# Optimization experiments

Hardware: AMD Instinct MI355X
Metric: run time of the kernel (lower is better)

Reference implementation:

```python
import jax, jax.numpy as jnp
import numpy as np

B, S, H, I = 2, 2048, 4096, 16384
EPS = 1e-12


def setup_inputs() -> dict:
    key = jax.random.key(0)
    ks = jax.random.split(key, 8)
    w_scale = 0.02
    return {
        "input": jax.random.normal(ks[0], (B, S, H), jnp.float32),
        "residual": jax.random.normal(ks[1], (B, S, H), jnp.float32),
        "bias": jax.random.normal(ks[2], (H,), jnp.float32) * w_scale,
        "attn_nw": jnp.ones((H,), jnp.float32),
        "attn_nb": jnp.zeros((H,), jnp.float32),
        "inter_w": jax.random.normal(ks[3], (I, H), jnp.float32) * w_scale,
        "inter_b": jax.random.normal(ks[4], (I,), jnp.float32) * w_scale,
        "output_w": jax.random.normal(ks[5], (H, I), jnp.float32) * w_scale,
        "output_b": jax.random.normal(ks[6], (H,), jnp.float32) * w_scale,
    }


def reference(input, residual, bias, attn_nw, attn_nb, inter_w, inter_b, output_w, output_b):
    # Fused mlp_gemm: residual_add = input + residual + attn-output bias
    residual_add = input + residual + bias  # [B,S,H]
    # LayerNorm over hidden dim with attn_nw/attn_nb
    mean = jnp.mean(residual_add, axis=-1, keepdims=True)
    var = jnp.var(residual_add, axis=-1, keepdims=True)
    ln = (residual_add - mean) * jax.lax.rsqrt(var + EPS) * attn_nw + attn_nb
    # Intermediate GEMM + bias + GELU (DeepSpeed uses tanh-approx gelu)
    inter = jax.nn.gelu(jnp.einsum("bsh,ih->bsi", ln, inter_w) + inter_b, approximate=True)
    # Output projection (vector_matmul)
    out = jnp.einsum("bsi,hi->bsh", inter, output_w)
    # bias_residual: add residual_add and output bias
    return out + residual_add + output_b
```

## Files before the change

### kernel.cpp

```cpp
#include <hip/hip_runtime.h>
#include <hip/hip_bf16.h>
#include <cstdint>
#include <math.h>

typedef __attribute__((ext_vector_type(4))) float f32x4;
typedef __attribute__((ext_vector_type(8))) __bf16 bf16x8;

__device__ __forceinline__ unsigned short f2bf(float f) {
    union { float f; unsigned u; } v; v.f = f;
    unsigned u = v.u + 0x7fffu + ((v.u >> 16) & 1u);
    return (unsigned short)(u >> 16);
}

__device__ __forceinline__ float gelu_tanh(float x) {
    float x3 = x * x * x;
    float t = tanhf(0.7978845608028654f * (x + 0.044715f * x3));
    return 0.5f * x * (1.0f + t);
}

__device__ __forceinline__ void gload_lds16(const void* g, void* l) {
    __builtin_amdgcn_global_load_lds(
        (__attribute__((address_space(1))) void*)(uintptr_t)g,
        (__attribute__((address_space(3))) void*)(unsigned)(uintptr_t)l,
        16, 0, 0);
}

__global__ __launch_bounds__(256)
void fused_add_ln(const float* __restrict__ in, const float* __restrict__ res,
                  const float* __restrict__ bias, const float* __restrict__ nw,
                  const float* __restrict__ nb, float* __restrict__ resadd,
                  unsigned short* __restrict__ lnout, int H) {
    const int row = blockIdx.x;
    const int tid = threadIdx.x;
    const size_t base = (size_t)row * H;
    float v[16];
    float s = 0.f, ss = 0.f;
#pragma unroll
    for (int i = 0; i < 4; ++i) {
        int idx = (i * 256 + tid) * 4;
        float4 a = *(const float4*)(in + base + idx);
        float4 b = *(const float4*)(res + base + idx);
        float4 c = *(const float4*)(bias + idx);
        float x0 = a.x + b.x + c.x, x1 = a.y + b.y + c.y;
        float x2 = a.z + b.z + c.z, x3 = a.w + b.w + c.w;
        v[i * 4 + 0] = x0; v[i * 4 + 1] = x1; v[i * 4 + 2] = x2; v[i * 4 + 3] = x3;
        s += x0 + x1 + x2 + x3;
        ss += x0 * x0 + x1 * x1 + x2 * x2 + x3 * x3;
    }
#pragma unroll
    for (int off = 32; off > 0; off >>= 1) {
        s += __shfl_down(s, off);
        ss += __shfl_down(ss, off);
    }
    __shared__ float red[8];
    const int w = tid >> 6;
    if ((tid & 63) == 0) { red[w] = s; red[4 + w] = ss; }
    __syncthreads();
    s = red[0] + red[1] + red[2] + red[3];
    ss = red[4] + red[5] + red[6] + red[7];
    const float mean = s / H;
    const float var = ss / H - mean * mean;
    const float rstd = rsqrtf(var + 1e-12f);
#pragma unroll
    for (int i = 0; i < 4; ++i) {
        int idx = (i * 256 + tid) * 4;
        float4 wv = *(const float4*)(nw + idx);
        float4 bv = *(const float4*)(nb + idx);
        float4 r;
        r.x = v[i * 4 + 0]; r.y = v[i * 4 + 1]; r.z = v[i * 4 + 2]; r.w = v[i * 4 + 3];
        *(float4*)(resadd + base + idx) = r;
        ushort4 o;
        o.x = f2bf((r.x - mean) * rstd * wv.x + bv.x);
        o.y = f2bf((r.y - mean) * rstd * wv.y + bv.y);
        o.z = f2bf((r.z - mean) * rstd * wv.z + bv.z);
        o.w = f2bf((r.w - mean) * rstd * wv.w + bv.w);
        *(ushort4*)(lnout + base + idx) = o;
    }
}

__global__ __launch_bounds__(256)
void cast_w(const float* __restrict__ w, unsigned short* __restrict__ o, long long n4) {
    long long i = (long long)blockIdx.x * 256 + threadIdx.x;
    if (i >= n4) return;
    float4 f = *(const float4*)(w + i * 4);
    ushort4 u;
    u.x = f2bf(f.x); u.y = f2bf(f.y); u.z = f2bf(f.z); u.w = f2bf(f.w);
    *(ushort4*)(o + i * 4) = u;
}

#define GBM 256
#define GBN 256
#define GBK 64

template <int EPI>
__global__ __launch_bounds__(512, 2)
void gemm256(const unsigned short* __restrict__ A,
             const unsigned short* __restrict__ B,
             const float* __restrict__ bias_n,
             const float* __restrict__ resadd,
             void* __restrict__ Cout,
             int M, int N, int K) {
    __shared__ unsigned short lds[2][2][GBM * GBK];
    const int tid = threadIdx.x;
    const int lane = tid & 63;
    const int w = tid >> 6;
    const int wr = w >> 2;
    const int wc = w & 3;

    const int nwg = gridDim.x;
    const int lg = (blockIdx.x & 7) * (nwg >> 3) + (blockIdx.x >> 3);
    const int nbx = N / GBN;
    const int brow = lg / nbx;
    const int bcol = lg % nbx;

    const int srow = tid >> 3;
    const int scol = ((((tid & 7) << 4) ^ ((srow & 7) << 4)) >> 1);
    const unsigned short* srcA = A + (size_t)(brow * GBM + srow) * K + scol;
    const unsigned short* srcB = B + (size_t)(bcol * GBN + srow) * K + scol;
    char* ldsBase = (char*)&lds[0][0][0];
    const int dOff = tid * 16;

    f32x4 acc[8][4] = {};

    const int NT = K / GBK;

#pragma unroll
    for (int c = 0; c < 4; ++c) {
        gload_lds16(srcA + (size_t)(c * 64) * K, ldsBase + c * 8192 + dOff);
        gload_lds16(srcB + (size_t)(c * 64) * K, ldsBase + 32768 + c * 8192 + dOff);
    }

    const int lrow = lane & 15;
    const int lswz = (lane & 7) << 4;
    const int lkx = (lane >> 4) << 4;

    for (int t = 0; t < NT; ++t) {
        const int cur = t & 1;
        if (t + 1 < NT) {
            const int kt = (t + 1) * GBK;
            char* dst = ldsBase + (cur ^ 1) * 65536;
#pragma unroll
            for (int c = 0; c < 4; ++c) {
                gload_lds16(srcA + (size_t)(c * 64) * K + kt, dst + c * 8192 + dOff);
                gload_lds16(srcB + (size_t)(c * 64) * K + kt, dst + 32768 + c * 8192 + dOff);
            }
            asm volatile("s_waitcnt vmcnt(8)" ::: "memory");
        } else {
            asm volatile("s_waitcnt vmcnt(0)" ::: "memory");
        }
        asm volatile("s_barrier" ::: "memory");

        const char* sA = (const char*)ldsBase + cur * 65536;
        const char* sB = sA + 32768;

        bf16x8 bq[4][2];
#pragma unroll
        for (int ni = 0; ni < 4; ++ni)
#pragma unroll
            for (int kk = 0; kk < 2; ++kk)
                bq[ni][kk] = *(const bf16x8*)(sB
                    + ((wc * 64 + ni * 16 + lrow) << 7)
                    + (((kk << 6) | lkx) ^ lswz));

#pragma unroll
        for (int q = 0; q < 4; ++q) {
            bf16x8 aq[2][2];
#pragma unroll
            for (int m2 = 0; m2 < 2; ++m2)
#pragma unroll
                for (int kk = 0; kk < 2; ++kk)
                    aq[m2][kk] = *(const bf16x8*)(sA
                        + ((wr * 128 + (q * 2 + m2) * 16 + lrow) << 7)
                        + (((kk << 6) | lkx) ^ lswz));
            asm volatile("s_waitcnt lgkmcnt(0)" ::: "memory");
            __builtin_amdgcn_sched_barrier(0);
            __builtin_amdgcn_s_setprio(1);
#pragma unroll
            for (int m2 = 0; m2 < 2; ++m2)
#pragma unroll
                for (int ni = 0; ni < 4; ++ni)
#pragma unroll
                    for (int kk = 0; kk < 2; ++kk)
                        acc[q * 2 + m2][ni] = __builtin_amdgcn_mfma_f32_16x16x32_bf16(
                            aq[m2][kk], bq[ni][kk], acc[q * 2 + m2][ni], 0, 0, 0);
            __builtin_amdgcn_s_setprio(0);
            asm volatile("s_barrier" ::: "memory");
        }
    }

    const int c0 = bcol * GBN + wc * 64 + lrow;
    const int r0 = brow * GBM + wr * 128 + (lane >> 4) * 4;
#pragma unroll
    for (int mi = 0; mi < 8; ++mi) {
#pragma unroll
        for (int j = 0; j < 4; ++j) {
            const int row = r0 + mi * 16 + j;
#pragma unroll
            for (int ni = 0; ni < 4; ++ni) {
                const int col = c0 + ni * 16;
                float x = acc[mi][ni][j] + bias_n[col];
                if (EPI == 0) {
                    ((unsigned short*)Cout)[(size_t)row * N + col] = f2bf(gelu_tanh(x));
                } else {
                    const size_t off = (size_t)row * N + col;
                    ((float*)Cout)[off] = x + resadd[off];
                }
            }
        }
    }
}

extern "C" void kernel_launch(void* const* d_in, const int* in_sizes, int n_in,
                              void* d_out, int out_size, void* d_ws, size_t ws_size,
                              hipStream_t stream) {
    const float* input    = (const float*)d_in[0];
    const float* residual = (const float*)d_in[1];
    const float* bias     = (const float*)d_in[2];
    const float* attn_nw  = (const float*)d_in[3];
    const float* attn_nb  = (const float*)d_in[4];
    const float* inter_w  = (const float*)d_in[5];
    const float* inter_b  = (const float*)d_in[6];
    const float* output_w = (const float*)d_in[7];
    const float* output_b = (const float*)d_in[8];

    const int H = in_sizes[3];
    const int I = in_sizes[6];
    const int T = in_sizes[0] / H;

    char* ws = (char*)d_ws;
    float* resadd      = (float*)ws;
    unsigned short* ln = (unsigned short*)(ws + (size_t)T * H * 4);
    unsigned short* w1 = (unsigned short*)((char*)ln + (size_t)T * H * 2);
    unsigned short* w2 = w1 + (size_t)I * H;
    unsigned short* act = w2 + (size_t)H * I;

    fused_add_ln<<<T, 256, 0, stream>>>(input, residual, bias, attn_nw, attn_nb,
                                        resadd, ln, H);

    {
        long long n4 = (long long)I * H / 4;
        int blocks = (int)((n4 + 255) / 256);
        cast_w<<<blocks, 256, 0, stream>>>(inter_w, w1, n4);
        cast_w<<<blocks, 256, 0, stream>>>(output_w, w2, n4);
    }

    {
        dim3 grid((T / GBM) * (I / GBN));
        gemm256<0><<<grid, 512, 0, stream>>>(ln, w1, inter_b, nullptr, act, T, I, H);
    }

    {
        dim3 grid((T / GBM) * (H / GBN));
        gemm256<1><<<grid, 512, 0, stream>>>(act, w2, output_b, resadd, d_out, T, H, I);
    }
}
```

Baseline: 1.285 ms.

## Software-pipeline GEMM main loop with interleaved half-tile staging and register double-buffering

Restructures the bf16 GEMM main loop into an 8-phase software pipeline. Each phase issues LDS fragment reads for the next MFMA group, streams a half-tile of the next K-step into LDS, and then runs MFMAs on fragments loaded in the previous phase. A and B fragments are double-buffered in registers, and global-to-LDS copies are split into finer stages gated by vmcnt(4). The goal is to hide LDS read latency and global load latency behind MFMA work and to remove the per-q lgkmcnt(0) stall. The cost is higher register pressure, more barriers per K-tile, and an assumption that NT is even.

```diff
diff --git a/kernel.cpp b/kernel.cpp
--- a/kernel.cpp
+++ b/kernel.cpp
@@ -92,6 +92,50 @@
 #define GBN 256
 #define GBK 64
 
+#define STAGE(s, mat, h, T) do {                                              \
+    const unsigned short* _src = ((mat) ? pB : pA)                            \
+        + (size_t)((h) * 128) * K + (size_t)(T) * 64;                         \
+    char* _dst = ldsc + (s) * 65536 + (mat) * 32768 + (h) * 16384 + dOff;     \
+    gload_lds16(_src, _dst);                                                  \
+    gload_lds16(_src + (size_t)64 * K, _dst + 8192);                          \
+} while (0)
+
+#define RD_B(tb, s) do {                                                      \
+    _Pragma("unroll")                                                         \
+    for (int ni = 0; ni < 4; ++ni)                                            \
+        _Pragma("unroll")                                                     \
+        for (int kk = 0; kk < 2; ++kk)                                        \
+            bq[tb][ni][kk] = *(const bf16x8*)(ldsc + (s) * 65536 + 32768      \
+                + ((wc * 64 + ni * 16 + lrow) << 7) + ckk[kk]);               \
+} while (0)
+
+#define RD_A(ab, q, s) do {                                                   \
+    _Pragma("unroll")                                                         \
+    for (int m2 = 0; m2 < 2; ++m2)                                            \
+        _Pragma("unroll")                                                     \
+        for (int kk = 0; kk < 2; ++kk)                                        \
+            aq[ab][m2][kk] = *(const bf16x8*)(ldsc + (s) * 65536              \
+                + ((wr * 128 + ((q) * 2 + m2) * 16 + lrow) << 7) + ckk[kk]);  \
+} while (0)
+
+#define MF(q, ab, tb) do {                                                    \
+    __builtin_amdgcn_s_setprio(1);                                            \
+    _Pragma("unroll")                                                         \
+    for (int m2 = 0; m2 < 2; ++m2)                                            \
+        _Pragma("unroll")                                                     \
+        for (int ni = 0; ni < 4; ++ni)                                        \
+            _Pragma("unroll")                                                 \
+            for (int kk = 0; kk < 2; ++kk)                                    \
+                acc[(q) * 2 + m2][ni] = __builtin_amdgcn_mfma_f32_16x16x32_bf16( \
+                    aq[ab][m2][kk], bq[tb][ni][kk], acc[(q) * 2 + m2][ni], 0, 0, 0); \
+    __builtin_amdgcn_s_setprio(0);                                            \
+} while (0)
+
+#define BAR do { asm volatile("s_barrier" ::: "memory");                      \
+                 __builtin_amdgcn_sched_barrier(0); } while (0)
+#define GATE4 asm volatile("s_waitcnt vmcnt(4)" ::: "memory")
+#define GATE0 asm volatile("s_waitcnt vmcnt(0)" ::: "memory")
+
 template <int EPI>
 __global__ __launch_bounds__(512, 2)
 void gemm256(const unsigned short* __restrict__ A,
@@ -100,7 +144,8 @@
              const float* __restrict__ resadd,
              void* __restrict__ Cout,
              int M, int N, int K) {
-    __shared__ unsigned short lds[2][2][GBM * GBK];
+    __shared__ unsigned short lds[2][2][2][128 * 64];
+    char* ldsc = (char*)&lds[0][0][0][0];
     const int tid = threadIdx.x;
     const int lane = tid & 63;
     const int w = tid >> 6;
@@ -115,77 +160,61 @@
 
     const int srow = tid >> 3;
     const int scol = ((((tid & 7) << 4) ^ ((srow & 7) << 4)) >> 1);
-    const unsigned short* srcA = A + (size_t)(brow * GBM + srow) * K + scol;
-    const unsigned short* srcB = B + (size_t)(bcol * GBN + srow) * K + scol;
-    char* ldsBase = (char*)&lds[0][0][0];
+    const unsigned short* pA = A + (size_t)(brow * GBM + srow) * K + scol;
+    const unsigned short* pB = B + (size_t)(bcol * GBN + srow) * K + scol;
     const int dOff = tid * 16;
 
+    const int lrow = lane & 15;
+    int ckk[2];
+    ckk[0] = (((lane >> 4) << 4)) ^ ((lrow & 7) << 4);
+    ckk[1] = ckk[0] ^ 64;
+
     f32x4 acc[8][4] = {};
+    bf16x8 aq[2][2][2];
+    bf16x8 bq[2][4][2];
+    {
+        bf16x8 z = {};
+#pragma unroll
+        for (int m2 = 0; m2 < 2; ++m2)
+#pragma unroll
+            for (int kk = 0; kk < 2; ++kk) aq[0][m2][kk] = z;
+#pragma unroll
+        for (int ni = 0; ni < 4; ++ni)
+#pragma unroll
+            for (int kk = 0; kk < 2; ++kk) bq[1][ni][kk] = z;
+    }
 
     const int NT = K / GBK;
-
-#pragma unroll
-    for (int c = 0; c < 4; ++c) {
-        gload_lds16(srcA + (size_t)(c * 64) * K, ldsBase + c * 8192 + dOff);
-        gload_lds16(srcB + (size_t)(c * 64) * K, ldsBase + 32768 + c * 8192 + dOff);
-    }
-
-    const int lrow = lane & 15;
-    const int lswz = (lane & 7) << 4;
-    const int lkx = (lane >> 4) << 4;
-
-    for (int t = 0; t < NT; ++t) {
-        const int cur = t & 1;
-        if (t + 1 < NT) {
-            const int kt = (t + 1) * GBK;
-            char* dst = ldsBase + (cur ^ 1) * 65536;
-#pragma unroll
-            for (int c = 0; c < 4; ++c) {
-                gload_lds16(srcA + (size_t)(c * 64) * K + kt, dst + c * 8192 + dOff);
-                gload_lds16(srcB + (size_t)(c * 64) * K + kt, dst + 32768 + c * 8192 + dOff);
-            }
-            asm volatile("s_waitcnt vmcnt(8)" ::: "memory");
-        } else {
-            asm volatile("s_waitcnt vmcnt(0)" ::: "memory");
-        }
-        asm volatile("s_barrier" ::: "memory");
-
-        const char* sA = (const char*)ldsBase + cur * 65536;
-        const char* sB = sA + 32768;
-
-        bf16x8 bq[4][2];
-#pragma unroll
-        for (int ni = 0; ni < 4; ++ni)
-#pragma unroll
-            for (int kk = 0; kk < 2; ++kk)
-                bq[ni][kk] = *(const bf16x8*)(sB
-                    + ((wc * 64 + ni * 16 + lrow) << 7)
-                    + (((kk << 6) | lkx) ^ lswz));
-
-#pragma unroll
-        for (int q = 0; q < 4; ++q) {
-            bf16x8 aq[2][2];
-#pragma unroll
-            for (int m2 = 0; m2 < 2; ++m2)
-#pragma unroll
-                for (int kk = 0; kk < 2; ++kk)
-                    aq[m2][kk] = *(const bf16x8*)(sA
-                        + ((wr * 128 + (q * 2 + m2) * 16 + lrow) << 7)
-                        + (((kk << 6) | lkx) ^ lswz));
-            asm volatile("s_waitcnt lgkmcnt(0)" ::: "memory");
-            __builtin_amdgcn_sched_barrier(0);
-            __builtin_amdgcn_s_setprio(1);
-#pragma unroll
-            for (int m2 = 0; m2 < 2; ++m2)
-#pragma unroll
-                for (int ni = 0; ni < 4; ++ni)
-#pragma unroll
-                    for (int kk = 0; kk < 2; ++kk)
-                        acc[q * 2 + m2][ni] = __builtin_amdgcn_mfma_f32_16x16x32_bf16(
-                            aq[m2][kk], bq[ni][kk], acc[q * 2 + m2][ni], 0, 0, 0);
-            __builtin_amdgcn_s_setprio(0);
-            asm volatile("s_barrier" ::: "memory");
-        }
+    const int niter = NT / 2;
+
+    STAGE(0, 1, 0, 0); STAGE(0, 1, 1, 0);
+    STAGE(0, 0, 0, 0); STAGE(0, 0, 1, 0);
+    STAGE(1, 1, 0, 1); STAGE(1, 1, 1, 1);
+    GATE4;
+    BAR;
+
+    for (int i = 0; i < niter - 1; ++i) {
+        const int T0 = 2 * i, T1 = 2 * i + 1;
+        RD_B(0, 0); RD_A(1, 0, 0); STAGE(1, 0, 0, T1);           BAR; MF(3, 0, 1);
+        RD_A(0, 1, 0);              STAGE(1, 0, 1, T1);          BAR; MF(0, 1, 0);
+        RD_A(1, 2, 0);              STAGE(0, 1, 0, T0 + 2);      BAR; MF(1, 0, 0);
+        RD_A(0, 3, 0);              STAGE(0, 1, 1, T0 + 2); GATE4; BAR; MF(2, 1, 0);
+        RD_B(1, 1); RD_A(1, 0, 1);  STAGE(0, 0, 0, T0 + 2);      BAR; MF(3, 0, 0);
+        RD_A(0, 1, 1);              STAGE(0, 0, 1, T0 + 2);      BAR; MF(0, 1, 1);
+        RD_A(1, 2, 1);              STAGE(1, 1, 0, T1 + 2);      BAR; MF(1, 0, 1);
+        RD_A(0, 3, 1);              STAGE(1, 1, 1, T1 + 2); GATE4; BAR; MF(2, 1, 1);
+    }
+    {
+        const int T1 = NT - 1;
+        RD_B(0, 0); RD_A(1, 0, 0); STAGE(1, 0, 0, T1);           BAR; MF(3, 0, 1);
+        RD_A(0, 1, 0);              STAGE(1, 0, 1, T1);          BAR; MF(0, 1, 0);
+        RD_A(1, 2, 0);                                           BAR; MF(1, 0, 0);
+        RD_A(0, 3, 0);                                     GATE0; BAR; MF(2, 1, 0);
+        RD_B(1, 1); RD_A(1, 0, 1);                               BAR; MF(3, 0, 0);
+        RD_A(0, 1, 1);                                           BAR; MF(0, 1, 1);
+        RD_A(1, 2, 1);                                           BAR; MF(1, 0, 1);
+        RD_A(0, 3, 1);                                           BAR; MF(2, 1, 1);
+        MF(3, 0, 1);
     }
 
     const int c0 = bcol * GBN + wc * 64 + lrow;
```

Result: slower. 3.226 ms (+151.1%).
